# Optimization experiments

Measured on AMD Instinct MI355X. Metric: run time of the kernel, lower is better.

Reference implementation:

```python
import jax, jax.numpy as jnp
import numpy as np

N_NODES = 50000
N_EDGES = 800000
C = 64          # node channels (in_dim == out_dim)
CE = 32         # edge channels
NEG_SLOPE = 0.2


def setup_inputs() -> dict:
    key = jax.random.key(0)
    k1, k2, k3, k4, k5 = jax.random.split(key, 5)
    x = jax.random.normal(k1, (N_NODES, C), dtype=jnp.float32)
    edge_index = jax.random.randint(k2, (2, N_EDGES), 0, N_NODES, dtype=jnp.int64)
    edge_attr = jax.random.normal(k3, (N_EDGES, CE), dtype=jnp.float32)
    # parameters (kaiming-uniform-ish scale)
    wn_bound = float(np.sqrt(6.0 / C))
    weight_node = jax.random.uniform(k4, (C, C), minval=-wn_bound, maxval=wn_bound, dtype=jnp.float32)
    wa_bound = float(np.sqrt(6.0 / (2 * C + CE)))
    weight_triplet_att = jax.random.uniform(k5, (1, 2 * C + CE), minval=-wa_bound, maxval=wa_bound, dtype=jnp.float32)
    bias = jnp.zeros((C,), dtype=jnp.float32)
    return {"x": x, "edge_index": edge_index, "edge_attr": edge_attr,
            "weight_node": weight_node, "weight_triplet_att": weight_triplet_att, "bias": bias}


def reference(x, edge_index, edge_attr, weight_node, weight_triplet_att, bias):
    # x: [N, C], edge_index: [2, E] (row 0 = source j, row 1 = target i), edge_attr: [E, Ce]
    n_nodes = x.shape[0]
    xw = x @ weight_node                      # [N, C]
    src, dst = edge_index[0], edge_index[1]
    x_j = xw[src]                             # [E, C] messages from source
    x_i = xw[dst]                             # [E, C] target features
    triplet = jnp.concatenate([x_i, edge_attr, x_j], axis=-1)   # [E, 2C+Ce]
    alpha = (triplet * weight_triplet_att).sum(axis=-1)          # [E]
    alpha = jax.nn.leaky_relu(alpha, NEG_SLOPE)
    # segment softmax over edges grouped by destination node (PyG softmax)
    seg_max = jax.ops.segment_max(alpha, dst, num_segments=n_nodes)  # [N]
    alpha = jnp.exp(alpha - seg_max[dst])
    seg_sum = jax.ops.segment_sum(alpha, dst, num_segments=n_nodes)  # [N]
    alpha = alpha / (seg_sum[dst] + 1e-16)
    msg = alpha[:, None] * x_j                                      # [E, C]
    out = jax.ops.segment_sum(msg, dst, num_segments=n_nodes)       # [N, C]
    return out + bias
```

## Files before the change

### kernel.cpp

```cpp
#include <hip/hip_runtime.h>
#include <math.h>

#define N_NODES 50000
#define N_EDGES 800000
#define C 64
#define CE 32
#define NEG_SLOPE 0.2f

#define SCAN_BLOCK 256
#define SCAN_ELEMS 4
#define SCAN_TILE (SCAN_BLOCK * SCAN_ELEMS)
#define SCAN_SHIFT 10
#define SCAN_NBLOCKS ((N_NODES + SCAN_TILE - 1) / SCAN_TILE)

__global__ __launch_bounds__(256) void k1_xw(
    const float* __restrict__ x, const float* __restrict__ W,
    const float* __restrict__ watt,
    float* __restrict__ xw, float* __restrict__ a_i, float* __restrict__ a_j)
{
    __shared__ float Wl[64 * 64];
    __shared__ float xs[4][64];
    int tid = threadIdx.x;
    for (int i = tid; i < 64 * 64 / 4; i += 256)
        ((float4*)Wl)[i] = ((const float4*)W)[i];
    int warp = tid >> 6, lane = tid & 63;
    int row = blockIdx.x * 4 + warp;
    if (row < N_NODES) xs[warp][lane] = x[(size_t)row * C + lane];
    __syncthreads();
    if (row >= N_NODES) return;
    float acc = 0.f;
#pragma unroll
    for (int k = 0; k < 64; k++) acc += xs[warp][k] * Wl[k * 64 + lane];
    xw[(size_t)row * C + lane] = acc;
    float vi = acc * watt[lane];
    float vj = acc * watt[96 + lane];
#pragma unroll
    for (int off = 32; off; off >>= 1) {
        vi += __shfl_down(vi, off, 64);
        vj += __shfl_down(vj, off, 64);
    }
    if (lane == 0) { a_i[row] = vi; a_j[row] = vj; }
}

__global__ __launch_bounds__(256) void k2_edge(
    const int* __restrict__ eidx, const float* __restrict__ edge_attr,
    const float* __restrict__ watt,
    const float* __restrict__ a_i, const float* __restrict__ a_j,
    float* __restrict__ wexp, unsigned* __restrict__ count,
    unsigned* __restrict__ erank)
{
    int e = blockIdx.x * 256 + threadIdx.x;
    if (e >= N_EDGES) return;
    int src = eidx[e];
    int dst = eidx[N_EDGES + e];
    const float4* ea = (const float4*)(edge_attr + (size_t)e * CE);
    float ec = 0.f;
#pragma unroll
    for (int k = 0; k < CE / 4; k++) {
        float4 v = ea[k];
        ec += v.x * watt[64 + 4 * k + 0] + v.y * watt[64 + 4 * k + 1] +
              v.z * watt[64 + 4 * k + 2] + v.w * watt[64 + 4 * k + 3];
    }
    float al = a_i[dst] + ec + a_j[src];
    al = al > 0.f ? al : NEG_SLOPE * al;
    wexp[e] = __expf(al);
    erank[e] = atomicAdd(&count[dst], 1u);
}

__global__ __launch_bounds__(SCAN_BLOCK) void k3a_blockscan(
    const unsigned* __restrict__ count, unsigned* __restrict__ base,
    unsigned* __restrict__ blocksum)
{
    __shared__ unsigned wsum[4];
    int tid = threadIdx.x, lane = tid & 63, warp = tid >> 6;
    int gbase = blockIdx.x * SCAN_TILE + tid * SCAN_ELEMS;
    unsigned v[SCAN_ELEMS];
    unsigned s = 0;
#pragma unroll
    for (int k = 0; k < SCAN_ELEMS; k++) {
        int i = gbase + k;
        v[k] = (i < N_NODES) ? count[i] : 0u;
        s += v[k];
    }
    unsigned inc = s;
#pragma unroll
    for (int off = 1; off < 64; off <<= 1) {
        unsigned t = __shfl_up(inc, off, 64);
        if (lane >= off) inc += t;
    }
    if (lane == 63) wsum[warp] = inc;
    __syncthreads();
    unsigned wpre = 0;
#pragma unroll
    for (int w = 0; w < 4; w++) if (w < warp) wpre += wsum[w];
    unsigned run = wpre + inc - s;
#pragma unroll
    for (int k = 0; k < SCAN_ELEMS; k++) {
        int i = gbase + k;
        if (i < N_NODES) base[i] = run;
        run += v[k];
    }
    if (tid == 255) blocksum[blockIdx.x] = wpre + inc;
}

__global__ __launch_bounds__(64) void k3b_scansums(unsigned* __restrict__ blocksum)
{
    int lane = threadIdx.x;
    unsigned v = (lane < SCAN_NBLOCKS) ? blocksum[lane] : 0u;
    unsigned inc = v;
#pragma unroll
    for (int off = 1; off < 64; off <<= 1) {
        unsigned t = __shfl_up(inc, off, 64);
        if (lane >= off) inc += t;
    }
    if (lane < SCAN_NBLOCKS) blocksum[lane] = inc - v;
}

__global__ __launch_bounds__(256) void k4_scatter(
    const int* __restrict__ eidx, const float* __restrict__ wexp,
    const unsigned* __restrict__ base, const unsigned* __restrict__ blocksum,
    const unsigned* __restrict__ erank, uint2* __restrict__ sorted)
{
    int e = blockIdx.x * 256 + threadIdx.x;
    if (e >= N_EDGES) return;
    int src = eidx[e];
    int dst = eidx[N_EDGES + e];
    unsigned pos = base[dst] + blocksum[(unsigned)dst >> SCAN_SHIFT] + erank[e];
    sorted[pos] = make_uint2((unsigned)src, __float_as_uint(wexp[e]));
}

__global__ __launch_bounds__(256) void k5_gather(
    const unsigned* __restrict__ base, const unsigned* __restrict__ blocksum,
    const unsigned* __restrict__ count, const uint2* __restrict__ sorted,
    const float* __restrict__ xw, const float* __restrict__ bias,
    float* __restrict__ out)
{
    int warp = threadIdx.x >> 6, lane = threadIdx.x & 63;
    int node = blockIdx.x * 4 + warp;
    if (node >= N_NODES) return;
    unsigned b = base[node] + blocksum[(unsigned)node >> SCAN_SHIFT];
    unsigned c = count[node];
    float acc = 0.f, wsum = 0.f;
    for (unsigned chunk = 0; chunk < c; chunk += 64) {
        unsigned m = min(64u, c - chunk);
        uint2 sw = make_uint2(0u, 0u);
        if (lane < m) sw = sorted[b + chunk + lane];
        for (unsigned t = 0; t < m; t++) {
            unsigned s = __shfl(sw.x, (int)t, 64);
            float w = __uint_as_float(__shfl(sw.y, (int)t, 64));
            wsum += w;
            acc += w * xw[(size_t)s * C + lane];
        }
    }
    float denom = wsum + 1e-16f;
    out[(size_t)node * C + lane] = acc / denom + bias[lane];
}

extern "C" void kernel_launch(void* const* d_in, const int* in_sizes, int n_in,
                              void* d_out, int out_size, void* d_ws, size_t ws_size,
                              hipStream_t stream) {
    const float* x         = (const float*)d_in[0];
    const int*   eidx      = (const int*)d_in[1];
    const float* edge_attr = (const float*)d_in[2];
    const float* W         = (const float*)d_in[3];
    const float* watt      = (const float*)d_in[4];
    const float* bias      = (const float*)d_in[5];
    float* out = (float*)d_out;

    char* ws = (char*)d_ws;
    size_t off = 0;
    auto alloc = [&](size_t bytes) -> void* {
        void* p = ws + off;
        off += (bytes + 255) & ~(size_t)255;
        return p;
    };
    float*    xw       = (float*)alloc((size_t)N_NODES * C * 4);
    float*    a_i      = (float*)alloc(N_NODES * 4);
    float*    a_j      = (float*)alloc(N_NODES * 4);
    float*    wexp     = (float*)alloc(N_EDGES * 4);
    unsigned* erank    = (unsigned*)alloc(N_EDGES * 4);
    uint2*    sorted   = (uint2*)alloc((size_t)N_EDGES * 8);
    unsigned* basep    = (unsigned*)alloc(N_NODES * 4);
    unsigned* blocksum = (unsigned*)alloc(SCAN_NBLOCKS * 4);
    unsigned* count    = (unsigned*)alloc(N_NODES * 4);

    hipMemsetAsync(count, 0, (size_t)N_NODES * 4, stream);

    k1_xw<<<(N_NODES + 3) / 4, 256, 0, stream>>>(x, W, watt, xw, a_i, a_j);
    k2_edge<<<(N_EDGES + 255) / 256, 256, 0, stream>>>(eidx, edge_attr, watt, a_i, a_j,
                                                       wexp, count, erank);
    k3a_blockscan<<<SCAN_NBLOCKS, SCAN_BLOCK, 0, stream>>>(count, basep, blocksum);
    k3b_scansums<<<1, 64, 0, stream>>>(blocksum);
    k4_scatter<<<(N_EDGES + 255) / 256, 256, 0, stream>>>(eidx, wexp, basep, blocksum,
                                                          erank, sorted);
    k5_gather<<<(N_NODES + 3) / 4, 256, 0, stream>>>(basep, blocksum, count, sorted,
                                                     xw, bias, out);
}
```

Baseline: 289.0 us.

## Store xw and edge weights in bf16, fuse scatter into edge kernel, vectorize gather

Stores the projected node features xw as bf16 and packs each edge's source index (16 bits) and bf16 softmax weight into a single 32-bit word. The edge pass is split into a histogram-only kernel and an edge kernel that computes the weight and scatters directly into CSR order through a cursor atomic, which removes the wexp/erank arrays and the separate scatter kernel. The gather kernel now has each wave process 8 edges at once, with 8-lane groups loading 16-byte bf16 rows and finishing with a cross-lane reduction. This lowers memory traffic in exchange for bf16 precision loss, and the 16-bit packing only holds while the node count stays below 65536.

```diff
diff --git a/kernel.cpp b/kernel.cpp
--- a/kernel.cpp
+++ b/kernel.cpp
@@ -13,10 +13,15 @@
 #define SCAN_SHIFT 10
 #define SCAN_NBLOCKS ((N_NODES + SCAN_TILE - 1) / SCAN_TILE)
 
+__device__ __forceinline__ unsigned bf16_rne(float f) {
+    unsigned u = __float_as_uint(f);
+    return (u + 0x7FFFu + ((u >> 16) & 1u)) >> 16;
+}
+
 __global__ __launch_bounds__(256) void k1_xw(
     const float* __restrict__ x, const float* __restrict__ W,
     const float* __restrict__ watt,
-    float* __restrict__ xw, float* __restrict__ a_i, float* __restrict__ a_j)
+    unsigned short* __restrict__ xwb, float* __restrict__ a_i, float* __restrict__ a_j)
 {
     __shared__ float Wl[64 * 64];
     __shared__ float xs[4][64];
@@ -31,7 +36,7 @@
     float acc = 0.f;
 #pragma unroll
     for (int k = 0; k < 64; k++) acc += xs[warp][k] * Wl[k * 64 + lane];
-    xw[(size_t)row * C + lane] = acc;
+    xwb[(size_t)row * C + lane] = (unsigned short)bf16_rne(acc);
     float vi = acc * watt[lane];
     float vj = acc * watt[96 + lane];
 #pragma unroll
@@ -42,12 +47,69 @@
     if (lane == 0) { a_i[row] = vi; a_j[row] = vj; }
 }
 
-__global__ __launch_bounds__(256) void k2_edge(
+__global__ __launch_bounds__(256) void k2a_hist(
+    const int* __restrict__ eidx, unsigned* __restrict__ count)
+{
+    int e = blockIdx.x * 256 + threadIdx.x;
+    if (e >= N_EDGES) return;
+    atomicAdd(&count[eidx[N_EDGES + e]], 1u);
+}
+
+__global__ __launch_bounds__(SCAN_BLOCK) void k3a_blockscan(
+    const unsigned* __restrict__ count, unsigned* __restrict__ base,
+    unsigned* __restrict__ blocksum)
+{
+    __shared__ unsigned wsum[4];
+    int tid = threadIdx.x, lane = tid & 63, warp = tid >> 6;
+    int gbase = blockIdx.x * SCAN_TILE + tid * SCAN_ELEMS;
+    unsigned v[SCAN_ELEMS];
+    unsigned s = 0;
+#pragma unroll
+    for (int k = 0; k < SCAN_ELEMS; k++) {
+        int i = gbase + k;
+        v[k] = (i < N_NODES) ? count[i] : 0u;
+        s += v[k];
+    }
+    unsigned inc = s;
+#pragma unroll
+    for (int off = 1; off < 64; off <<= 1) {
+        unsigned t = __shfl_up(inc, off, 64);
+        if (lane >= off) inc += t;
+    }
+    if (lane == 63) wsum[warp] = inc;
+    __syncthreads();
+    unsigned wpre = 0;
+#pragma unroll
+    for (int w = 0; w < 4; w++) if (w < warp) wpre += wsum[w];
+    unsigned run = wpre + inc - s;
+#pragma unroll
+    for (int k = 0; k < SCAN_ELEMS; k++) {
+        int i = gbase + k;
+        if (i < N_NODES) base[i] = run;
+        run += v[k];
+    }
+    if (tid == 255) blocksum[blockIdx.x] = wpre + inc;
+}
+
+__global__ __launch_bounds__(64) void k3b_scansums(unsigned* __restrict__ blocksum)
+{
+    int lane = threadIdx.x;
+    unsigned v = (lane < SCAN_NBLOCKS) ? blocksum[lane] : 0u;
+    unsigned inc = v;
+#pragma unroll
+    for (int off = 1; off < 64; off <<= 1) {
+        unsigned t = __shfl_up(inc, off, 64);
+        if (lane >= off) inc += t;
+    }
+    if (lane < SCAN_NBLOCKS) blocksum[lane] = inc - v;
+}
+
+__global__ __launch_bounds__(256) void k2b_edge(
     const int* __restrict__ eidx, const float* __restrict__ edge_attr,
     const float* __restrict__ watt,
     const float* __restrict__ a_i, const float* __restrict__ a_j,
-    float* __restrict__ wexp, unsigned* __restrict__ count,
-    unsigned* __restrict__ erank)
+    const unsigned* __restrict__ base, const unsigned* __restrict__ blocksum,
+    unsigned* __restrict__ cursor, unsigned* __restrict__ sorted)
 {
     int e = blockIdx.x * 256 + threadIdx.x;
     if (e >= N_EDGES) return;
@@ -63,97 +125,71 @@
     }
     float al = a_i[dst] + ec + a_j[src];
     al = al > 0.f ? al : NEG_SLOPE * al;
-    wexp[e] = __expf(al);
-    erank[e] = atomicAdd(&count[dst], 1u);
-}
-
-__global__ __launch_bounds__(SCAN_BLOCK) void k3a_blockscan(
-    const unsigned* __restrict__ count, unsigned* __restrict__ base,
-    unsigned* __restrict__ blocksum)
-{
-    __shared__ unsigned wsum[4];
-    int tid = threadIdx.x, lane = tid & 63, warp = tid >> 6;
-    int gbase = blockIdx.x * SCAN_TILE + tid * SCAN_ELEMS;
-    unsigned v[SCAN_ELEMS];
-    unsigned s = 0;
-#pragma unroll
-    for (int k = 0; k < SCAN_ELEMS; k++) {
-        int i = gbase + k;
-        v[k] = (i < N_NODES) ? count[i] : 0u;
-        s += v[k];
-    }
-    unsigned inc = s;
-#pragma unroll
-    for (int off = 1; off < 64; off <<= 1) {
-        unsigned t = __shfl_up(inc, off, 64);
-        if (lane >= off) inc += t;
-    }
-    if (lane == 63) wsum[warp] = inc;
-    __syncthreads();
-    unsigned wpre = 0;
-#pragma unroll
-    for (int w = 0; w < 4; w++) if (w < warp) wpre += wsum[w];
-    unsigned run = wpre + inc - s;
-#pragma unroll
-    for (int k = 0; k < SCAN_ELEMS; k++) {
-        int i = gbase + k;
-        if (i < N_NODES) base[i] = run;
-        run += v[k];
-    }
-    if (tid == 255) blocksum[blockIdx.x] = wpre + inc;
-}
-
-__global__ __launch_bounds__(64) void k3b_scansums(unsigned* __restrict__ blocksum)
-{
-    int lane = threadIdx.x;
-    unsigned v = (lane < SCAN_NBLOCKS) ? blocksum[lane] : 0u;
-    unsigned inc = v;
-#pragma unroll
-    for (int off = 1; off < 64; off <<= 1) {
-        unsigned t = __shfl_up(inc, off, 64);
-        if (lane >= off) inc += t;
-    }
-    if (lane < SCAN_NBLOCKS) blocksum[lane] = inc - v;
-}
-
-__global__ __launch_bounds__(256) void k4_scatter(
-    const int* __restrict__ eidx, const float* __restrict__ wexp,
-    const unsigned* __restrict__ base, const unsigned* __restrict__ blocksum,
-    const unsigned* __restrict__ erank, uint2* __restrict__ sorted)
-{
-    int e = blockIdx.x * 256 + threadIdx.x;
-    if (e >= N_EDGES) return;
-    int src = eidx[e];
-    int dst = eidx[N_EDGES + e];
-    unsigned pos = base[dst] + blocksum[(unsigned)dst >> SCAN_SHIFT] + erank[e];
-    sorted[pos] = make_uint2((unsigned)src, __float_as_uint(wexp[e]));
+    float w = __expf(al);
+    unsigned pk = ((unsigned)src << 16) | bf16_rne(w);
+    unsigned pos = base[dst] + blocksum[(unsigned)dst >> SCAN_SHIFT]
+                 + atomicAdd(&cursor[dst], 1u);
+    sorted[pos] = pk;
 }
 
 __global__ __launch_bounds__(256) void k5_gather(
     const unsigned* __restrict__ base, const unsigned* __restrict__ blocksum,
-    const unsigned* __restrict__ count, const uint2* __restrict__ sorted,
-    const float* __restrict__ xw, const float* __restrict__ bias,
+    const unsigned* __restrict__ count, const unsigned* __restrict__ sorted,
+    const unsigned short* __restrict__ xwb, const float* __restrict__ bias,
     float* __restrict__ out)
 {
     int warp = threadIdx.x >> 6, lane = threadIdx.x & 63;
     int node = blockIdx.x * 4 + warp;
     if (node >= N_NODES) return;
+    int group = lane >> 3, sub = lane & 7;
     unsigned b = base[node] + blocksum[(unsigned)node >> SCAN_SHIFT];
     unsigned c = count[node];
-    float acc = 0.f, wsum = 0.f;
+    float acc[8];
+#pragma unroll
+    for (int i = 0; i < 8; i++) acc[i] = 0.f;
+    float wpart = 0.f;
     for (unsigned chunk = 0; chunk < c; chunk += 64) {
         unsigned m = min(64u, c - chunk);
-        uint2 sw = make_uint2(0u, 0u);
-        if (lane < m) sw = sorted[b + chunk + lane];
-        for (unsigned t = 0; t < m; t++) {
-            unsigned s = __shfl(sw.x, (int)t, 64);
-            float w = __uint_as_float(__shfl(sw.y, (int)t, 64));
-            wsum += w;
-            acc += w * xw[(size_t)s * C + lane];
+        unsigned pk = 0u;
+        if (lane < m) pk = sorted[b + chunk + lane];
+        wpart += __uint_as_float(pk << 16);
+        unsigned iters = (m + 7) >> 3;
+        for (unsigned it = 0; it < iters; it++) {
+            int t = (int)(it * 8) + group;
+            unsigned p = (unsigned)__shfl((int)pk, t, 64);
+            float w = __uint_as_float(p << 16);
+            unsigned s = p >> 16;
+            uint4 v = ((const uint4*)(xwb + (size_t)s * C))[sub];
+            acc[0] += w * __uint_as_float(v.x << 16);
+            acc[1] += w * __uint_as_float(v.x & 0xFFFF0000u);
+            acc[2] += w * __uint_as_float(v.y << 16);
+            acc[3] += w * __uint_as_float(v.y & 0xFFFF0000u);
+            acc[4] += w * __uint_as_float(v.z << 16);
+            acc[5] += w * __uint_as_float(v.z & 0xFFFF0000u);
+            acc[6] += w * __uint_as_float(v.w << 16);
+            acc[7] += w * __uint_as_float(v.w & 0xFFFF0000u);
         }
     }
-    float denom = wsum + 1e-16f;
-    out[(size_t)node * C + lane] = acc / denom + bias[lane];
+#pragma unroll
+    for (int off = 8; off < 64; off <<= 1) {
+#pragma unroll
+        for (int i = 0; i < 8; i++) acc[i] += __shfl_xor(acc[i], off, 64);
+    }
+#pragma unroll
+    for (int off = 1; off < 64; off <<= 1)
+        wpart += __shfl_xor(wpart, off, 64);
+    float rden = 1.0f / (wpart + 1e-16f);
+    if (group == 0) {
+        float4 b4a = ((const float4*)bias)[sub * 2];
+        float4 b4b = ((const float4*)bias)[sub * 2 + 1];
+        float4 o1, o2;
+        o1.x = acc[0] * rden + b4a.x; o1.y = acc[1] * rden + b4a.y;
+        o1.z = acc[2] * rden + b4a.z; o1.w = acc[3] * rden + b4a.w;
+        o2.x = acc[4] * rden + b4b.x; o2.y = acc[5] * rden + b4b.y;
+        o2.z = acc[6] * rden + b4b.z; o2.w = acc[7] * rden + b4b.w;
+        ((float4*)(out + (size_t)node * C))[sub * 2] = o1;
+        ((float4*)(out + (size_t)node * C))[sub * 2 + 1] = o2;
+    }
 }
 
 extern "C" void kernel_launch(void* const* d_in, const int* in_sizes, int n_in,
@@ -174,25 +210,24 @@
         off += (bytes + 255) & ~(size_t)255;
         return p;
     };
-    float*    xw       = (float*)alloc((size_t)N_NODES * C * 4);
+    unsigned short* xwb    = (unsigned short*)alloc((size_t)N_NODES * C * 2);
     float*    a_i      = (float*)alloc(N_NODES * 4);
     float*    a_j      = (float*)alloc(N_NODES * 4);
-    float*    wexp     = (float*)alloc(N_EDGES * 4);
-    unsigned* erank    = (unsigned*)alloc(N_EDGES * 4);
-    uint2*    sorted   = (uint2*)alloc((size_t)N_EDGES * 8);
+    unsigned* sorted   = (unsigned*)alloc((size_t)N_EDGES * 4);
     unsigned* basep    = (unsigned*)alloc(N_NODES * 4);
     unsigned* blocksum = (unsigned*)alloc(SCAN_NBLOCKS * 4);
-    unsigned* count    = (unsigned*)alloc(N_NODES * 4);
-
-    hipMemsetAsync(count, 0, (size_t)N_NODES * 4, stream);
-
-    k1_xw<<<(N_NODES + 3) / 4, 256, 0, stream>>>(x, W, watt, xw, a_i, a_j);
-    k2_edge<<<(N_EDGES + 255) / 256, 256, 0, stream>>>(eidx, edge_attr, watt, a_i, a_j,
-                                                       wexp, count, erank);
+    void* zero_region = (void*)(ws + off);
+    unsigned* count  = (unsigned*)alloc(N_NODES * 4);
+    unsigned* cursor = (unsigned*)alloc(N_NODES * 4);
+
+    hipMemsetAsync(zero_region, 0, (size_t)(ws + off - (char*)zero_region), stream);
+
+    k1_xw<<<(N_NODES + 3) / 4, 256, 0, stream>>>(x, W, watt, xwb, a_i, a_j);
+    k2a_hist<<<(N_EDGES + 255) / 256, 256, 0, stream>>>(eidx, count);
     k3a_blockscan<<<SCAN_NBLOCKS, SCAN_BLOCK, 0, stream>>>(count, basep, blocksum);
     k3b_scansums<<<1, 64, 0, stream>>>(blocksum);
-    k4_scatter<<<(N_EDGES + 255) / 256, 256, 0, stream>>>(eidx, wexp, basep, blocksum,
-                                                          erank, sorted);
+    k2b_edge<<<(N_EDGES + 255) / 256, 256, 0, stream>>>(eidx, edge_attr, watt, a_i, a_j,
+                                                        basep, blocksum, cursor, sorted);
     k5_gather<<<(N_NODES + 3) / 4, 256, 0, stream>>>(basep, blocksum, count, sorted,
-                                                     xw, bias, out);
-}
+                                                     xwb, bias, out);
+}
```

Measured after the change: 297.0 us. +2.8%, slower.
